# Performance work log

Hardware: AMD Instinct MI355X
Metric: run time of the kernel (lower is better)

The kernel has to match this reference:

```python
import jax, jax.numpy as jnp
import numpy as np

G, NPG = 8192, 8            # graphs, nodes per graph (8 sensors, recon head = 8*9)
N = G * NPG                 # 65536 total nodes
IN, HID, HEADS = 9, 64, 4
NEG_SLOPE = 0.2


def _fc_edges():
    # directed fully-connected edges (no self loops) within each 8-node graph
    i, j = np.meshgrid(np.arange(NPG), np.arange(NPG), indexing='ij')
    m = i != j
    src_l, dst_l = i[m], j[m]                       # 56 edges per graph
    off = (np.arange(G) * NPG)[:, None]
    src = (off + src_l[None, :]).ravel()
    dst = (off + dst_l[None, :]).ravel()
    return np.stack([src, dst]).astype(np.int32)    # [2, 458752]


def setup_inputs() -> dict:
    key = jax.random.key(0)
    ks = jax.random.split(key, 30)
    ei = jnp.asarray(_fc_edges())
    E = ei.shape[1]
    p = lambda k, shape, s=0.1: jax.random.normal(ks[k], shape, jnp.float32) * s
    return {
        'x': jax.random.normal(ks[0], (N, IN), jnp.float32),
        'edge_index': ei,
        'edge_weight': jax.random.uniform(ks[1], (E,), jnp.float32),
        'batch': jnp.repeat(jnp.arange(G, dtype=jnp.int32), NPG),
        'W1': p(2, (IN, HEADS * HID)), 'a_src1': p(3, (HEADS, HID)),
        'a_dst1': p(4, (HEADS, HID)), 'We1': p(5, (1, HEADS * HID)),
        'a_e1': p(6, (HEADS, HID)), 'b1': jnp.zeros((HEADS * HID,), jnp.float32),
        'W2': p(7, (HEADS * HID, HID)), 'a_src2': p(8, (1, HID)),
        'a_dst2': p(9, (1, HID)), 'We2': p(10, (1, HID)),
        'a_e2': p(11, (1, HID)), 'b2': jnp.zeros((HID,), jnp.float32),
        # recon head: 64 -> 128 -> 72
        'Wr1': p(12, (HID, 2 * HID)), 'br1': jnp.zeros((2 * HID,), jnp.float32),
        'Wr2': p(13, (2 * HID, 8 * IN)), 'br2': jnp.zeros((8 * IN,), jnp.float32),
        # classify head: 64 -> 32 -> 1
        'Wc1': p(14, (HID, 32)), 'bc1': jnp.zeros((32,), jnp.float32),
        'Wc2': p(15, (32, 1)), 'bc2': jnp.zeros((1,), jnp.float32),
    }


def _gat_conv(x, edge_index, edge_attr, W, a_src, a_dst, We, a_e, bias):
    """PyG GATConv (eval mode): add_self_loops(fill='mean'), edge_dim features."""
    n = x.shape[0]
    heads, ch = a_src.shape
    src, dst = edge_index[0], edge_index[1]
    # self loops with edge_attr = mean of incoming edge_attr per node
    deg = jax.ops.segment_sum(jnp.ones_like(edge_attr[:, :1]), dst, num_segments=n)
    loop_attr = jax.ops.segment_sum(edge_attr, dst, num_segments=n) / jnp.maximum(deg, 1.0)
    src = jnp.concatenate([src, jnp.arange(n, dtype=src.dtype)])
    dst = jnp.concatenate([dst, jnp.arange(n, dtype=dst.dtype)])
    ea = jnp.concatenate([edge_attr, loop_attr], axis=0)          # [E+N, 1]
    xp = (x @ W).reshape(n, heads, ch)                            # [N, H, C]
    al_s = jnp.einsum('nhc,hc->nh', xp, a_src)
    al_d = jnp.einsum('nhc,hc->nh', xp, a_dst)
    ep = (ea @ We).reshape(-1, heads, ch)                         # [E+N, H, C]
    al_e = jnp.einsum('ehc,hc->eh', ep, a_e)
    alpha = al_s[src] + al_d[dst] + al_e                          # [E+N, H]
    alpha = jax.nn.leaky_relu(alpha, NEG_SLOPE)
    # segment softmax over destination nodes
    m = jax.ops.segment_max(alpha, dst, num_segments=n)
    alpha = jnp.exp(alpha - m[dst])
    s = jax.ops.segment_sum(alpha, dst, num_segments=n)
    alpha = alpha / (s[dst] + 1e-16)
    # scatter-aggregate weighted messages
    out = jax.ops.segment_sum(xp[src] * alpha[..., None], dst, num_segments=n)
    return out.reshape(n, heads * ch) + bias


def reference(x, edge_index, edge_weight, batch,
              W1, a_src1, a_dst1, We1, a_e1, b1,
              W2, a_src2, a_dst2, We2, a_e2, b2,
              Wr1, br1, Wr2, br2, Wc1, bc1, Wc2, bc2):
    ew = edge_weight[:, None]
    h = _gat_conv(x, edge_index, ew, W1, a_src1, a_dst1, We1, a_e1, b1)
    h = jax.nn.elu(h)
    h = _gat_conv(h, edge_index, ew, W2, a_src2, a_dst2, We2, a_e2, b2)
    h = jax.nn.elu(h)
    # global mean pool over graphs
    g = G
    cnt = jax.ops.segment_sum(jnp.ones((h.shape[0], 1), h.dtype), batch, num_segments=g)
    emb = jax.ops.segment_sum(h, batch, num_segments=g) / jnp.maximum(cnt, 1.0)
    recon = jax.nn.relu(emb @ Wr1 + br1) @ Wr2 + br2
    cls = jax.nn.relu(emb @ Wc1 + bc1) @ Wc2 + bc2
    return recon, cls
```

## Files before the change

kernel.cpp:

```cpp
#include <hip/hip_runtime.h>
#include <math.h>

#define NEG 0.2f
#define GROUPS 8192

typedef unsigned short u16;
typedef u16 ushort8 __attribute__((ext_vector_type(8)));
typedef short s16x8 __attribute__((ext_vector_type(8)));
typedef float f32x4 __attribute__((ext_vector_type(4)));

#define WFENCE() asm volatile("s_waitcnt lgkmcnt(0)" ::: "memory")

__device__ __forceinline__ float lrelu(float x){ return x >= 0.f ? x : NEG*x; }
__device__ __forceinline__ float eluf(float x){ return x > 0.f ? x : __expf(x) - 1.f; }
__device__ __forceinline__ int eidx(int s,int d){ return s*7 + (d<s ? d : d-1); }
__device__ __forceinline__ float bf2f(u16 u){
    union { unsigned i; float f; } v; v.i = ((unsigned)u)<<16; return v.f;
}
__device__ __forceinline__ u16 f2bf(float f){
    union { float f; unsigned i; } v; v.f = f;
    unsigned r = v.i + 0x7fffu + ((v.i>>16)&1u);
    return (u16)(r>>16);
}

__global__ __launch_bounds__(64)
void prep(const float* __restrict__ W1, const float* __restrict__ a_src1,
          const float* __restrict__ a_dst1, const float* __restrict__ W2,
          const float* __restrict__ Wr1, const float* __restrict__ Wr2,
          const float* __restrict__ Wc1,
          const float* __restrict__ We1, const float* __restrict__ a_e1,
          const float* __restrict__ We2, const float* __restrict__ a_e2,
          u16* __restrict__ wfrag, u16* __restrict__ wr1f,
          u16* __restrict__ wr2f, u16* __restrict__ wc1f,
          float* __restrict__ w1s, float* __restrict__ ces)
{
    const int b = blockIdx.x, l = threadIdx.x;
    const int c0 = l & 15, o = l >> 4;
    if (b < 32) {
        const int t = b >> 3, s = b & 7;
        ushort8 p;
#pragma unroll
        for (int j = 0; j < 8; ++j) p[j] = f2bf(W2[(s*32 + o*8 + j)*64 + t*16 + c0]);
        *(ushort8*)(wfrag + (size_t)(b*64 + l)*8) = p;
    } else if (b < 48) {
        const int f = b - 32, ks = f >> 3, t = f & 7;
        ushort8 p;
#pragma unroll
        for (int j = 0; j < 8; ++j) p[j] = f2bf(Wr1[(ks*32 + o*8 + j)*128 + t*16 + c0]);
        *(ushort8*)(wr1f + (size_t)(f*64 + l)*8) = p;
    } else if (b < 68) {
        const int f = b - 48, ks = f / 5, t = f % 5;
        const int c = t*16 + c0;
        ushort8 p;
#pragma unroll
        for (int j = 0; j < 8; ++j)
            p[j] = (c < 72) ? f2bf(Wr2[(ks*32 + o*8 + j)*72 + c]) : (u16)0;
        *(ushort8*)(wr2f + (size_t)(f*64 + l)*8) = p;
    } else if (b < 72) {
        const int f = b - 68, ks = f >> 1, t = f & 1;
        ushort8 p;
#pragma unroll
        for (int j = 0; j < 8; ++j) p[j] = f2bf(Wc1[(ks*32 + o*8 + j)*32 + t*16 + c0]);
        *(ushort8*)(wc1f + (size_t)(f*64 + l)*8) = p;
    } else if (b == 72) {
        for (int idx = l; idx < 72; idx += 64) {
            const int k = idx >> 3, cc = idx & 7, h = cc & 3;
            const float* av = (cc < 4) ? a_src1 : a_dst1;
            float acc = 0.f;
#pragma unroll 8
            for (int i = 0; i < 64; ++i) acc = fmaf(W1[k*256 + h*64 + i], av[h*64 + i], acc);
            w1s[idx] = acc;
        }
    } else {
        if (l < 4) {
            float c = 0.f;
#pragma unroll 8
            for (int i = 0; i < 64; ++i) c = fmaf(We1[l*64+i], a_e1[l*64+i], c);
            ces[l] = c;
        } else if (l == 4) {
            float c = 0.f;
#pragma unroll 8
            for (int i = 0; i < 64; ++i) c = fmaf(We2[i], a_e2[i], c);
            ces[4] = c;
        }
    }
}

__global__ __launch_bounds__(64, 4)
void gat_fused5(const float* __restrict__ x, const float* __restrict__ ew_g,
    const float* __restrict__ W1, const float* __restrict__ b1,
    const float* __restrict__ a_src2, const float* __restrict__ a_dst2,
    const float* __restrict__ b2,
    const float* __restrict__ br1, const float* __restrict__ br2,
    const float* __restrict__ bc1, const float* __restrict__ Wc2,
    const float* __restrict__ bc2,
    const u16* __restrict__ wfrag, const u16* __restrict__ wr1f,
    const u16* __restrict__ wr2f, const u16* __restrict__ wc1f,
    const float* __restrict__ w1s, const float* __restrict__ cesg,
    float* __restrict__ recon, float* __restrict__ cls)
{
    __shared__ __align__(16) u16 act[2][8][264];
    __shared__ __align__(16) float alpha1f[2][4][8][8];
    __shared__ float als2[2][8], ald2[2][8];
    __shared__ float alpha2[2][8][8];
    __shared__ float ews2[2][56];
    __shared__ float lws[2][8];

    u16* const embs16 = (u16*)alpha1f;
    u16* const r1s16  = (u16*)alpha1f + 128;

    const int lane = threadIdx.x;
    const int n    = lane >> 3;
    const int cg   = lane & 7;
    const int g0   = blockIdx.x * 2;

    {
        const float* eg = ew_g + (size_t)g0 * 56;
        for (int i = lane; i < 112; i += 64) (&ews2[0][0])[i] = eg[i];
    }

    float xr0[9], xr1[9];
    {
        const float* p0 = x + (size_t)g0 * 72 + n * 9;
        const float* p1 = p0 + 72;
#pragma unroll
        for (int k = 0; k < 9; ++k) { xr0[k] = p0[k]; xr1[k] = p1[k]; }
    }

    float alsv = 0.f, aldv = 0.f;
    {
        const int gg = lane >> 5, nn = (lane >> 2) & 7, hh = lane & 3;
        const float* xs = x + (size_t)(g0 + gg) * 72 + nn * 9;
#pragma unroll
        for (int k = 0; k < 9; ++k) {
            const float xv = xs[k];
            alsv = fmaf(xv, w1s[k*8 + hh], alsv);
            aldv = fmaf(xv, w1s[k*8 + 4 + hh], aldv);
        }
    }

    WFENCE();

    if (lane < 16) {
        const int g = lane >> 3, d = lane & 7;
        float s = 0.f;
#pragma unroll
        for (int ss = 0; ss < 8; ++ss) if (ss != d) s += ews2[g][eidx(ss, d)];
        lws[g][d] = s * (1.f/7.f);
    }

    {
#pragma unroll
        for (int u = 0; u < 4; ++u) {
            const int cb = u*64 + cg*8;
            float a0[8] = {0,0,0,0,0,0,0,0}, a1[8] = {0,0,0,0,0,0,0,0};
#pragma unroll
            for (int k = 0; k < 9; ++k) {
                const float4 w0 = *(const float4*)(W1 + k*256 + cb);
                const float4 w1 = *(const float4*)(W1 + k*256 + cb + 4);
                const float f0 = xr0[k], f1 = xr1[k];
                a0[0]=fmaf(f0,w0.x,a0[0]); a0[1]=fmaf(f0,w0.y,a0[1]);
                a0[2]=fmaf(f0,w0.z,a0[2]); a0[3]=fmaf(f0,w0.w,a0[3]);
                a0[4]=fmaf(f0,w1.x,a0[4]); a0[5]=fmaf(f0,w1.y,a0[5]);
                a0[6]=fmaf(f0,w1.z,a0[6]); a0[7]=fmaf(f0,w1.w,a0[7]);
                a1[0]=fmaf(f1,w0.x,a1[0]); a1[1]=fmaf(f1,w0.y,a1[1]);
                a1[2]=fmaf(f1,w0.z,a1[2]); a1[3]=fmaf(f1,w0.w,a1[3]);
                a1[4]=fmaf(f1,w1.x,a1[4]); a1[5]=fmaf(f1,w1.y,a1[5]);
                a1[6]=fmaf(f1,w1.z,a1[6]); a1[7]=fmaf(f1,w1.w,a1[7]);
            }
            ushort8 p0, p1;
#pragma unroll
            for (int j = 0; j < 8; ++j) { p0[j] = f2bf(a0[j]); p1[j] = f2bf(a1[j]); }
            *(ushort8*)&act[0][n][cb] = p0;
            *(ushort8*)&act[1][n][cb] = p1;
        }
    }

    WFENCE();

    {
        const int gg = lane >> 5, dd = (lane >> 2) & 7, hh = lane & 3;
        const float ce = cesg[hh];
        const float ad = aldv;
        float lg[8], mx = -1e30f;
#pragma unroll
        for (int ss = 0; ss < 8; ++ss) {
            const float as_ = __shfl(alsv, (lane & 0x23) | (ss << 2));
            const float w = (ss == dd) ? lws[gg][dd] : ews2[gg][eidx(ss, dd)];
            float t = as_ + ad + ce * w;
            t = lrelu(t);
            lg[ss] = t; mx = fmaxf(mx, t);
        }
        float sum = 0.f;
#pragma unroll
        for (int ss = 0; ss < 8; ++ss) { lg[ss] = __expf(lg[ss] - mx); sum += lg[ss]; }
        const float inv = 1.f / (sum + 1e-16f);
#pragma unroll
        for (int ss = 0; ss < 8; ++ss) alpha1f[gg][hh][dd][ss] = lg[ss] * inv;
    }

    WFENCE();

    for (int g = 0; g < 2; ++g) {
        float hv[32];
#pragma unroll
        for (int u = 0; u < 4; ++u) {
            const float4 al0 = *(const float4*)&alpha1f[g][u][n][0];
            const float4 al1 = *(const float4*)&alpha1f[g][u][n][4];
            float acc[8] = {0,0,0,0,0,0,0,0};
#pragma unroll
            for (int s = 0; s < 8; ++s) {
                const float av = (s==0)?al0.x:(s==1)?al0.y:(s==2)?al0.z:(s==3)?al0.w:
                                 (s==4)?al1.x:(s==5)?al1.y:(s==6)?al1.z:al1.w;
                const ushort8 v = *(const ushort8*)&act[g][s][u*64 + cg*8];
#pragma unroll
                for (int j = 0; j < 8; ++j) acc[j] = fmaf(av, bf2f(v[j]), acc[j]);
            }
#pragma unroll
            for (int j = 0; j < 8; ++j) hv[u*8+j] = acc[j];
        }
        WFENCE();
#pragma unroll
        for (int u = 0; u < 4; ++u) {
            const int cb = u*64 + cg*8;
            const float4 b0 = *(const float4*)(b1 + cb);
            const float4 b2v = *(const float4*)(b1 + cb + 4);
            ushort8 p;
            p[0]=f2bf(eluf(hv[u*8+0]+b0.x)); p[1]=f2bf(eluf(hv[u*8+1]+b0.y));
            p[2]=f2bf(eluf(hv[u*8+2]+b0.z)); p[3]=f2bf(eluf(hv[u*8+3]+b0.w));
            p[4]=f2bf(eluf(hv[u*8+4]+b2v.x)); p[5]=f2bf(eluf(hv[u*8+5]+b2v.y));
            p[6]=f2bf(eluf(hv[u*8+6]+b2v.z)); p[7]=f2bf(eluf(hv[u*8+7]+b2v.w));
            *(ushort8*)&act[g][n][cb] = p;
        }
        WFENCE();
    }

    f32x4 acc[4] = {{0,0,0,0},{0,0,0,0},{0,0,0,0},{0,0,0,0}};
    {
        const int r = lane & 15;
        const u16* arow = &act[r >> 3][r & 7][(lane >> 4) * 8];
#pragma unroll
        for (int s = 0; s < 8; ++s) {
            const s16x8 af = *(const s16x8*)(arow + s * 32);
#pragma unroll
            for (int t = 0; t < 4; ++t) {
                const s16x8 bf = *(const s16x8*)(wfrag + (size_t)(((t*8 + s)*64 + lane))*8);
                acc[t] = __builtin_amdgcn_mfma_f32_16x16x32_bf16(af, bf, acc[t], 0, 0, 0);
            }
        }
    }

    {
        const int c0 = lane & 15;
        float sp[4] = {0,0,0,0}, dp[4] = {0,0,0,0};
#pragma unroll
        for (int t = 0; t < 4; ++t) {
            const float as_ = a_src2[t*16 + c0];
            const float ad_ = a_dst2[t*16 + c0];
#pragma unroll
            for (int i = 0; i < 4; ++i) {
                sp[i] = fmaf(acc[t][i], as_, sp[i]);
                dp[i] = fmaf(acc[t][i], ad_, dp[i]);
            }
        }
#pragma unroll
        for (int i = 0; i < 4; ++i) {
            sp[i] += __shfl_xor(sp[i],1); sp[i] += __shfl_xor(sp[i],2);
            sp[i] += __shfl_xor(sp[i],4); sp[i] += __shfl_xor(sp[i],8);
            dp[i] += __shfl_xor(dp[i],1); dp[i] += __shfl_xor(dp[i],2);
            dp[i] += __shfl_xor(dp[i],4); dp[i] += __shfl_xor(dp[i],8);
        }
        if ((lane & 15) == 0) {
            const int rb = (lane >> 4) * 4;
#pragma unroll
            for (int i = 0; i < 4; ++i) {
                const int r = rb + i;
                als2[r >> 3][r & 7] = sp[i];
                ald2[r >> 3][r & 7] = dp[i];
            }
        }
    }
    WFENCE();

    float* xf0 = reinterpret_cast<float*>(&act[0][0][0]);
    float* xf1 = reinterpret_cast<float*>(&act[1][0][0]);
    {
        const int c0 = lane & 15;
#pragma unroll
        for (int t = 0; t < 4; ++t)
#pragma unroll
            for (int i = 0; i < 4; ++i) {
                const int r = (lane >> 4)*4 + i;
                float* xf = (r >> 3) ? xf1 : xf0;
                xf[(r & 7)*68 + t*16 + c0] = acc[t][i];
            }
    }
    WFENCE();

    if (lane < 16) {
        const int g = lane >> 3, d = lane & 7;
        const float ce = cesg[4], ad = ald2[g][d];
        float lg[8], mx = -1e30f;
#pragma unroll
        for (int ss = 0; ss < 8; ++ss) {
            const float w = (ss == d) ? lws[g][d] : ews2[g][eidx(ss, d)];
            float t = als2[g][ss] + ad + ce * w;
            t = lrelu(t);
            lg[ss] = t; mx = fmaxf(mx, t);
        }
        float sum = 0.f;
#pragma unroll
        for (int ss = 0; ss < 8; ++ss) { lg[ss] = __expf(lg[ss] - mx); sum += lg[ss]; }
        const float inv = 1.f / (sum + 1e-16f);
#pragma unroll
        for (int ss = 0; ss < 8; ++ss) alpha2[g][d][ss] = lg[ss] * inv;
    }
    WFENCE();

    float h2[2][8];
#pragma unroll
    for (int g = 0; g < 2; ++g) {
        const float* xf = g ? xf1 : xf0;
        float a[8] = {0,0,0,0,0,0,0,0};
#pragma unroll
        for (int ss = 0; ss < 8; ++ss) {
            const float av = alpha2[g][n][ss];
            const float4 v0 = *(const float4*)(xf + ss*68 + cg*8);
            const float4 v1 = *(const float4*)(xf + ss*68 + cg*8 + 4);
            a[0]=fmaf(av,v0.x,a[0]); a[1]=fmaf(av,v0.y,a[1]);
            a[2]=fmaf(av,v0.z,a[2]); a[3]=fmaf(av,v0.w,a[3]);
            a[4]=fmaf(av,v1.x,a[4]); a[5]=fmaf(av,v1.y,a[5]);
            a[6]=fmaf(av,v1.z,a[6]); a[7]=fmaf(av,v1.w,a[7]);
        }
        const float4 b0 = *(const float4*)(b2 + cg*8);
        const float4 b1v = *(const float4*)(b2 + cg*8 + 4);
        h2[g][0]=eluf(a[0]+b0.x); h2[g][1]=eluf(a[1]+b0.y);
        h2[g][2]=eluf(a[2]+b0.z); h2[g][3]=eluf(a[3]+b0.w);
        h2[g][4]=eluf(a[4]+b1v.x); h2[g][5]=eluf(a[5]+b1v.y);
        h2[g][6]=eluf(a[6]+b1v.z); h2[g][7]=eluf(a[7]+b1v.w);
    }
#pragma unroll
    for (int g = 0; g < 2; ++g)
#pragma unroll
        for (int j = 0; j < 8; ++j) {
            float v = h2[g][j];
            v += __shfl_xor(v, 8); v += __shfl_xor(v, 16); v += __shfl_xor(v, 32);
            h2[g][j] = v * 0.125f;
        }
    if (n == 0) {
#pragma unroll
        for (int g = 0; g < 2; ++g) {
            ushort8 p;
#pragma unroll
            for (int j = 0; j < 8; ++j) p[j] = f2bf(h2[g][j]);
            *(ushort8*)&embs16[g*64 + lane*8] = p;
        }
    }
    WFENCE();

    s16x8 aemb0 = {0,0,0,0,0,0,0,0}, aemb1 = {0,0,0,0,0,0,0,0};
    {
        const int r = lane & 15, o = lane >> 4;
        if (r < 2) {
            aemb0 = *(const s16x8*)&embs16[r*64 + o*8];
            aemb1 = *(const s16x8*)&embs16[r*64 + 32 + o*8];
        }
    }
    {
        f32x4 ar[8];
        const f32x4 z = {0,0,0,0};
#pragma unroll
        for (int t = 0; t < 8; ++t) ar[t] = z;
#pragma unroll
        for (int t = 0; t < 8; ++t) {
            ar[t] = __builtin_amdgcn_mfma_f32_16x16x32_bf16(
                aemb0, *(const s16x8*)(wr1f + (size_t)((0*8 + t)*64 + lane)*8), ar[t], 0,0,0);
            ar[t] = __builtin_amdgcn_mfma_f32_16x16x32_bf16(
                aemb1, *(const s16x8*)(wr1f + (size_t)((1*8 + t)*64 + lane)*8), ar[t], 0,0,0);
        }
        const int c0 = lane & 15, o = lane >> 4;
        if (o == 0) {
#pragma unroll
            for (int t = 0; t < 8; ++t) {
                const float bb = br1[t*16 + c0];
                r1s16[0*128 + t*16 + c0] = f2bf(fmaxf(ar[t][0] + bb, 0.f));
                r1s16[1*128 + t*16 + c0] = f2bf(fmaxf(ar[t][1] + bb, 0.f));
            }
        }
    }
    WFENCE();

    {
        f32x4 ac[5];
        const f32x4 z = {0,0,0,0};
#pragma unroll
        for (int t = 0; t < 5; ++t) ac[t] = z;
        const int r = lane & 15, o = lane >> 4;
#pragma unroll
        for (int ks = 0; ks < 4; ++ks) {
            s16x8 a = {0,0,0,0,0,0,0,0};
            if (r < 2) a = *(const s16x8*)&r1s16[r*128 + ks*32 + o*8];
#pragma unroll
            for (int t = 0; t < 5; ++t)
                ac[t] = __builtin_amdgcn_mfma_f32_16x16x32_bf16(
                    a, *(const s16x8*)(wr2f + (size_t)((ks*5 + t)*64 + lane)*8), ac[t], 0,0,0);
        }
        if (o == 0) {
            const int c0 = r;
#pragma unroll
            for (int t = 0; t < 5; ++t) {
                const int c = t*16 + c0;
                if (c < 72) {
                    const float bb = br2[c];
                    recon[(size_t)g0*72 + c]       = ac[t][0] + bb;
                    recon[(size_t)(g0+1)*72 + c]   = ac[t][1] + bb;
                }
            }
        }
    }

    {
        f32x4 ac[2];
        const f32x4 z = {0,0,0,0};
        ac[0] = z; ac[1] = z;
#pragma unroll
        for (int t = 0; t < 2; ++t) {
            ac[t] = __builtin_amdgcn_mfma_f32_16x16x32_bf16(
                aemb0, *(const s16x8*)(wc1f + (size_t)((0*2 + t)*64 + lane)*8), ac[t], 0,0,0);
            ac[t] = __builtin_amdgcn_mfma_f32_16x16x32_bf16(
                aemb1, *(const s16x8*)(wc1f + (size_t)((1*2 + t)*64 + lane)*8), ac[t], 0,0,0);
        }
        const int c0 = lane & 15;
        const float bb0 = bc1[c0], bb1 = bc1[16 + c0];
        const float wc0 = Wc2[c0], wc1v = Wc2[16 + c0];
        float p0 = fmaxf(ac[0][0] + bb0, 0.f)*wc0 + fmaxf(ac[1][0] + bb1, 0.f)*wc1v;
        float p1 = fmaxf(ac[0][1] + bb0, 0.f)*wc0 + fmaxf(ac[1][1] + bb1, 0.f)*wc1v;
        p0 += __shfl_xor(p0,1); p0 += __shfl_xor(p0,2); p0 += __shfl_xor(p0,4); p0 += __shfl_xor(p0,8);
        p1 += __shfl_xor(p1,1); p1 += __shfl_xor(p1,2); p1 += __shfl_xor(p1,4); p1 += __shfl_xor(p1,8);
        if (lane == 0) { cls[g0] = p0 + bc2[0]; cls[g0+1] = p1 + bc2[0]; }
    }
}

extern "C" void kernel_launch(void* const* d_in, const int* in_sizes, int n_in,
                              void* d_out, int out_size, void* d_ws, size_t ws_size,
                              hipStream_t stream) {
    const float* x      = (const float*)d_in[0];
    const float* ew     = (const float*)d_in[2];
    const float* W1     = (const float*)d_in[4];
    const float* a_src1 = (const float*)d_in[5];
    const float* a_dst1 = (const float*)d_in[6];
    const float* We1    = (const float*)d_in[7];
    const float* a_e1   = (const float*)d_in[8];
    const float* b1     = (const float*)d_in[9];
    const float* W2     = (const float*)d_in[10];
    const float* a_src2 = (const float*)d_in[11];
    const float* a_dst2 = (const float*)d_in[12];
    const float* We2    = (const float*)d_in[13];
    const float* a_e2   = (const float*)d_in[14];
    const float* b2     = (const float*)d_in[15];
    const float* Wr1    = (const float*)d_in[16];
    const float* br1    = (const float*)d_in[17];
    const float* Wr2    = (const float*)d_in[18];
    const float* br2    = (const float*)d_in[19];
    const float* Wc1    = (const float*)d_in[20];
    const float* bc1    = (const float*)d_in[21];
    const float* Wc2    = (const float*)d_in[22];
    const float* bc2    = (const float*)d_in[23];

    float* recon = (float*)d_out;
    float* cls   = (float*)d_out + (size_t)GROUPS * 72;

    char* ws = (char*)d_ws;
    u16*   wfrag = (u16*)(ws + 0);
    u16*   wr1f  = (u16*)(ws + 32768);
    u16*   wr2f  = (u16*)(ws + 49152);
    u16*   wc1f  = (u16*)(ws + 69632);
    float* w1s   = (float*)(ws + 73728);
    float* ces   = (float*)(ws + 74016);

    hipLaunchKernelGGL(prep, dim3(74), dim3(64), 0, stream,
                       W1, a_src1, a_dst1, W2, Wr1, Wr2, Wc1,
                       We1, a_e1, We2, a_e2,
                       wfrag, wr1f, wr2f, wc1f, w1s, ces);

    hipLaunchKernelGGL(gat_fused5, dim3(GROUPS/2), dim3(64), 0, stream,
                       x, ew, W1, b1, a_src2, a_dst2, b2,
                       br1, br2, bc1, Wc2, bc2,
                       wfrag, wr1f, wr2f, wc1f, w1s, ces,
                       recon, cls);
}
```

Baseline: 54.93 us.

## Use barriers, bf16 attention weights, and register-shuffle layer-2 softmax

Replaces the inline lgkmcnt fences with __syncthreads barriers, which are safer for a single-wave block and may let the compiler order LDS accesses better. Attention coefficients for both layers are now stored in shared memory as packed bf16 vectors instead of fp32, so each read is one 16-byte load. The layer-2 softmax is computed from shuffled register values across all lanes rather than staged through shared memory by 16 lanes, which removes one LDS round trip and one fence. In exchange, the attention weights lose precision, and an extra barrier is added before the embedding store.

```diff
diff --git a/kernel.cpp b/kernel.cpp
--- a/kernel.cpp
+++ b/kernel.cpp
@@ -8,8 +8,6 @@
 typedef u16 ushort8 __attribute__((ext_vector_type(8)));
 typedef short s16x8 __attribute__((ext_vector_type(8)));
 typedef float f32x4 __attribute__((ext_vector_type(4)));
-
-#define WFENCE() asm volatile("s_waitcnt lgkmcnt(0)" ::: "memory")
 
 __device__ __forceinline__ float lrelu(float x){ return x >= 0.f ? x : NEG*x; }
 __device__ __forceinline__ float eluf(float x){ return x > 0.f ? x : __expf(x) - 1.f; }
@@ -87,7 +85,7 @@
 }
 
 __global__ __launch_bounds__(64, 4)
-void gat_fused5(const float* __restrict__ x, const float* __restrict__ ew_g,
+void gat_fused7(const float* __restrict__ x, const float* __restrict__ ew_g,
     const float* __restrict__ W1, const float* __restrict__ b1,
     const float* __restrict__ a_src2, const float* __restrict__ a_dst2,
     const float* __restrict__ b2,
@@ -100,14 +98,13 @@
     float* __restrict__ recon, float* __restrict__ cls)
 {
     __shared__ __align__(16) u16 act[2][8][264];
-    __shared__ __align__(16) float alpha1f[2][4][8][8];
-    __shared__ float als2[2][8], ald2[2][8];
-    __shared__ float alpha2[2][8][8];
+    __shared__ __align__(16) u16 alpha1b[2][4][8][8];
+    __shared__ __align__(16) u16 alpha2b[2][8][8];
     __shared__ float ews2[2][56];
     __shared__ float lws[2][8];
 
-    u16* const embs16 = (u16*)alpha1f;
-    u16* const r1s16  = (u16*)alpha1f + 128;
+    u16* const embs16 = (u16*)alpha1b;
+    u16* const r1s16  = (u16*)alpha1b + 128;
 
     const int lane = threadIdx.x;
     const int n    = lane >> 3;
@@ -139,7 +136,7 @@
         }
     }
 
-    WFENCE();
+    __syncthreads();
 
     if (lane < 16) {
         const int g = lane >> 3, d = lane & 7;
@@ -176,7 +173,7 @@
         }
     }
 
-    WFENCE();
+    __syncthreads();
 
     {
         const int gg = lane >> 5, dd = (lane >> 2) & 7, hh = lane & 3;
@@ -195,23 +192,23 @@
 #pragma unroll
         for (int ss = 0; ss < 8; ++ss) { lg[ss] = __expf(lg[ss] - mx); sum += lg[ss]; }
         const float inv = 1.f / (sum + 1e-16f);
-#pragma unroll
-        for (int ss = 0; ss < 8; ++ss) alpha1f[gg][hh][dd][ss] = lg[ss] * inv;
-    }
-
-    WFENCE();
+        ushort8 ap;
+#pragma unroll
+        for (int ss = 0; ss < 8; ++ss) ap[ss] = f2bf(lg[ss] * inv);
+        *(ushort8*)&alpha1b[gg][hh][dd][0] = ap;
+    }
+
+    __syncthreads();
 
     for (int g = 0; g < 2; ++g) {
         float hv[32];
 #pragma unroll
         for (int u = 0; u < 4; ++u) {
-            const float4 al0 = *(const float4*)&alpha1f[g][u][n][0];
-            const float4 al1 = *(const float4*)&alpha1f[g][u][n][4];
+            const ushort8 al8 = *(const ushort8*)&alpha1b[g][u][n][0];
             float acc[8] = {0,0,0,0,0,0,0,0};
 #pragma unroll
             for (int s = 0; s < 8; ++s) {
-                const float av = (s==0)?al0.x:(s==1)?al0.y:(s==2)?al0.z:(s==3)?al0.w:
-                                 (s==4)?al1.x:(s==5)?al1.y:(s==6)?al1.z:al1.w;
+                const float av = bf2f(al8[s]);
                 const ushort8 v = *(const ushort8*)&act[g][s][u*64 + cg*8];
 #pragma unroll
                 for (int j = 0; j < 8; ++j) acc[j] = fmaf(av, bf2f(v[j]), acc[j]);
@@ -219,7 +216,7 @@
 #pragma unroll
             for (int j = 0; j < 8; ++j) hv[u*8+j] = acc[j];
         }
-        WFENCE();
+        __syncthreads();
 #pragma unroll
         for (int u = 0; u < 4; ++u) {
             const int cb = u*64 + cg*8;
@@ -232,7 +229,7 @@
             p[6]=f2bf(eluf(hv[u*8+6]+b2v.z)); p[7]=f2bf(eluf(hv[u*8+7]+b2v.w));
             *(ushort8*)&act[g][n][cb] = p;
         }
-        WFENCE();
+        __syncthreads();
     }
 
     f32x4 acc[4] = {{0,0,0,0},{0,0,0,0},{0,0,0,0},{0,0,0,0}};
@@ -250,9 +247,9 @@
         }
     }
 
+    float sp[4] = {0,0,0,0}, dp[4] = {0,0,0,0};
     {
         const int c0 = lane & 15;
-        float sp[4] = {0,0,0,0}, dp[4] = {0,0,0,0};
 #pragma unroll
         for (int t = 0; t < 4; ++t) {
             const float as_ = a_src2[t*16 + c0];
@@ -270,17 +267,39 @@
             dp[i] += __shfl_xor(dp[i],1); dp[i] += __shfl_xor(dp[i],2);
             dp[i] += __shfl_xor(dp[i],4); dp[i] += __shfl_xor(dp[i],8);
         }
-        if ((lane & 15) == 0) {
-            const int rb = (lane >> 4) * 4;
-#pragma unroll
-            for (int i = 0; i < 4; ++i) {
-                const int r = rb + i;
-                als2[r >> 3][r & 7] = sp[i];
-                ald2[r >> 3][r & 7] = dp[i];
-            }
-        }
-    }
-    WFENCE();
+    }
+
+    {
+        const int g = (lane >> 3) & 1, d = lane & 7;
+        float al[8];
+#pragma unroll
+        for (int ss = 0; ss < 8; ++ss)
+            al[ss] = __shfl(sp[ss & 3], (g*2 + (ss >> 2)) * 16);
+        const int srcd = (g*2 + (d >> 2)) * 16;
+        const float q0 = __shfl(dp[0], srcd), q1 = __shfl(dp[1], srcd);
+        const float q2 = __shfl(dp[2], srcd), q3 = __shfl(dp[3], srcd);
+        const float ad = (d & 2) ? ((d & 1) ? q3 : q2) : ((d & 1) ? q1 : q0);
+        const float ce = cesg[4];
+        float lg[8], mx = -1e30f;
+#pragma unroll
+        for (int ss = 0; ss < 8; ++ss) {
+            const float w = (ss == d) ? lws[g][d] : ews2[g][eidx(ss, d)];
+            float t = al[ss] + ad + ce * w;
+            t = lrelu(t);
+            lg[ss] = t; mx = fmaxf(mx, t);
+        }
+        float sum = 0.f;
+#pragma unroll
+        for (int ss = 0; ss < 8; ++ss) { lg[ss] = __expf(lg[ss] - mx); sum += lg[ss]; }
+        const float inv = 1.f / (sum + 1e-16f);
+        if (lane < 16) {
+            ushort8 ap;
+#pragma unroll
+            for (int ss = 0; ss < 8; ++ss) ap[ss] = f2bf(lg[ss] * inv);
+            *(ushort8*)&alpha2b[g][d][0] = ap;
+        }
+    }
+    __syncthreads();
 
     float* xf0 = reinterpret_cast<float*>(&act[0][0][0]);
     float* xf1 = reinterpret_cast<float*>(&act[1][0][0]);
@@ -295,36 +314,17 @@
                 xf[(r & 7)*68 + t*16 + c0] = acc[t][i];
             }
     }
-    WFENCE();
-
-    if (lane < 16) {
-        const int g = lane >> 3, d = lane & 7;
-        const float ce = cesg[4], ad = ald2[g][d];
-        float lg[8], mx = -1e30f;
-#pragma unroll
-        for (int ss = 0; ss < 8; ++ss) {
-            const float w = (ss == d) ? lws[g][d] : ews2[g][eidx(ss, d)];
-            float t = als2[g][ss] + ad + ce * w;
-            t = lrelu(t);
-            lg[ss] = t; mx = fmaxf(mx, t);
-        }
-        float sum = 0.f;
-#pragma unroll
-        for (int ss = 0; ss < 8; ++ss) { lg[ss] = __expf(lg[ss] - mx); sum += lg[ss]; }
-        const float inv = 1.f / (sum + 1e-16f);
-#pragma unroll
-        for (int ss = 0; ss < 8; ++ss) alpha2[g][d][ss] = lg[ss] * inv;
-    }
-    WFENCE();
+    __syncthreads();
 
     float h2[2][8];
 #pragma unroll
     for (int g = 0; g < 2; ++g) {
         const float* xf = g ? xf1 : xf0;
+        const ushort8 a2 = *(const ushort8*)&alpha2b[g][n][0];
         float a[8] = {0,0,0,0,0,0,0,0};
 #pragma unroll
         for (int ss = 0; ss < 8; ++ss) {
-            const float av = alpha2[g][n][ss];
+            const float av = bf2f(a2[ss]);
             const float4 v0 = *(const float4*)(xf + ss*68 + cg*8);
             const float4 v1 = *(const float4*)(xf + ss*68 + cg*8 + 4);
             a[0]=fmaf(av,v0.x,a[0]); a[1]=fmaf(av,v0.y,a[1]);
@@ -347,6 +347,7 @@
             v += __shfl_xor(v, 8); v += __shfl_xor(v, 16); v += __shfl_xor(v, 32);
             h2[g][j] = v * 0.125f;
         }
+    __syncthreads();
     if (n == 0) {
 #pragma unroll
         for (int g = 0; g < 2; ++g) {
@@ -356,7 +357,7 @@
             *(ushort8*)&embs16[g*64 + lane*8] = p;
         }
     }
-    WFENCE();
+    __syncthreads();
 
     s16x8 aemb0 = {0,0,0,0,0,0,0,0}, aemb1 = {0,0,0,0,0,0,0,0};
     {
@@ -388,7 +389,7 @@
             }
         }
     }
-    WFENCE();
+    __syncthreads();
 
     {
         f32x4 ac[5];
@@ -483,7 +484,7 @@
                        We1, a_e1, We2, a_e2,
                        wfrag, wr1f, wr2f, wc1f, w1s, ces);
 
-    hipLaunchKernelGGL(gat_fused5, dim3(GROUPS/2), dim3(64), 0, stream,
+    hipLaunchKernelGGL(gat_fused7, dim3(GROUPS/2), dim3(64), 0, stream,
                        x, ew, W1, b1, a_src2, a_dst2, b2,
                        br1, br2, bc1, Wc2, bc2,
                        wfrag, wr1f, wr2f, wc1f, w1s, ces,
```

Result: slower. 60.29 us (+9.8%).
